# Optimization experiments

Measured on AMD Instinct MI355X. Metric: run time of the kernel, lower is better.

## Reference

```python
import jax, jax.numpy as jnp
import numpy as np

EMBED = 256
HEADS = 8
LEVELS = 4
POINTS = 8
CAMS = 6
D_HEAD = EMBED // HEADS  # 32
SHAPES = [(92, 160), (46, 80), (23, 40), (12, 20)]  # (H, W) per level, L = 19560


def setup_inputs() -> dict:
    key = jax.random.key(0)
    ks = jax.random.split(key, 12)
    bs, nq, Z = 1, 2500, 4
    L = sum(h * w for h, w in SHAPES)

    def lin(k, fan_in, fan_out, scale=1.0):
        return jax.random.normal(k, (fan_in, fan_out), jnp.float32) * (scale / np.sqrt(fan_in).astype(np.float32))

    return dict(
        query=jax.random.normal(ks[0], (bs, nq, EMBED), jnp.float32),
        key_feats=jax.random.normal(ks[1], (CAMS, L, bs, EMBED), jnp.float32),
        reference_points_cam=jax.random.uniform(ks[2], (CAMS, bs, nq, Z, 2), jnp.float32),
        bev_mask=jax.random.bernoulli(ks[3], 0.3, (CAMS, bs, nq, Z)),
        spatial_shapes=jnp.array(SHAPES, dtype=jnp.int32),
        W_value=lin(ks[4], EMBED, EMBED),
        b_value=jnp.zeros((EMBED,), jnp.float32),
        W_off=lin(ks[5], EMBED, HEADS * LEVELS * POINTS * 2, 0.1),
        b_off=jnp.zeros((HEADS * LEVELS * POINTS * 2,), jnp.float32),
        W_attn=lin(ks[6], EMBED, HEADS * LEVELS * POINTS),
        b_attn=jnp.zeros((HEADS * LEVELS * POINTS,), jnp.float32),
        W_out=lin(ks[7], EMBED, EMBED),
        b_out=jnp.zeros((EMBED,), jnp.float32),
    )


def _deform_attn(q, val, ref, W_off, b_off, W_attn, b_attn):
    """MSDeformableAttention3D core. q: (Bc,Nq,C), val: (Bc,L,H,d) [already value-projected],
    ref: (Bc,Nq,Z,2) normalized camera-plane points."""
    Bc, Nq, C = q.shape
    Z = ref.shape[2]
    # sampling offsets, normalized per level by (W, H)
    off = (q @ W_off + b_off).reshape(Bc, Nq, HEADS, LEVELS, POINTS, 2)
    norm = jnp.array([[w, h] for h, w in SHAPES], jnp.float32)  # (Lv, 2) as (W, H)
    off = off / norm[None, None, None, :, None, :]
    # BEVFormer 3D combination: broadcast offsets over the Z pillar anchors
    off = off.reshape(Bc, Nq, HEADS, LEVELS, POINTS // Z, Z, 2)
    loc = ref[:, :, None, None, None, :, :] + off  # (Bc,Nq,H,Lv,P/Z,Z,2)
    loc = loc.reshape(Bc, Nq, HEADS, LEVELS, POINTS, 2)
    # attention weights softmaxed jointly over (levels*points)
    aw = jax.nn.softmax((q @ W_attn + b_attn).reshape(Bc, Nq, HEADS, LEVELS * POINTS), axis=-1)
    aw = aw.reshape(Bc, Nq, HEADS, LEVELS, POINTS)

    val_t = val.transpose(0, 2, 1, 3)  # (Bc,H,L,d)
    gather = jax.vmap(jax.vmap(lambda vm, im: vm[im]))  # over Bc and H
    out = jnp.zeros((Bc, HEADS, Nq, D_HEAD), jnp.float32)
    start = 0
    for lvl, (Hh, Ww) in enumerate(SHAPES):
        v_l = val_t[:, :, start:start + Hh * Ww]  # (Bc,H,HW,d)
        start += Hh * Ww
        # grid_sample semantics, align_corners=False, zero padding
        x = loc[:, :, :, lvl, :, 0] * Ww - 0.5  # (Bc,Nq,H,P)
        y = loc[:, :, :, lvl, :, 1] * Hh - 0.5
        x0 = jnp.floor(x)
        y0 = jnp.floor(y)
        fx = x - x0
        fy = y - y0
        a_l = aw[:, :, :, lvl]  # (Bc,Nq,H,P)
        for dy in (0, 1):
            for dx in (0, 1):
                xi = x0 + dx
                yi = y0 + dy
                wgt = (fx if dx else 1.0 - fx) * (fy if dy else 1.0 - fy)
                valid = (xi >= 0) & (xi < Ww) & (yi >= 0) & (yi < Hh)
                idx = (jnp.clip(yi, 0, Hh - 1) * Ww + jnp.clip(xi, 0, Ww - 1)).astype(jnp.int32)
                cw = jnp.where(valid, wgt * a_l, 0.0).transpose(0, 2, 1, 3)  # (Bc,H,Nq,P)
                g = gather(v_l, idx.transpose(0, 2, 1, 3))  # (Bc,H,Nq,P,d)
                out = out + jnp.einsum('bhnp,bhnpd->bhnd', cw, g)
    return out.transpose(0, 2, 1, 3).reshape(Bc, Nq, C)


def reference(query, key_feats, reference_points_cam, bev_mask, spatial_shapes,
              W_value, b_value, W_off, b_off, W_attn, b_attn, W_out, b_out):
    bs, nq, C = query.shape
    # Rebatch equivalent: every camera sees all queries; invalid ones are masked out
    # after the (fully per-query) deformable attention, which matches the original
    # gather->pad->attend->scatter math exactly.
    q_bc = jnp.broadcast_to(query[:, None], (bs, CAMS, nq, C)).reshape(bs * CAMS, nq, C)
    v = key_feats.transpose(2, 0, 1, 3).reshape(bs * CAMS, -1, C)  # (Bc,L,C)
    val = (v @ W_value + b_value).reshape(bs * CAMS, -1, HEADS, D_HEAD)
    ref = reference_points_cam.transpose(1, 0, 2, 3, 4).reshape(bs * CAMS, nq, -1, 2)
    out = _deform_attn(q_bc, val, ref, W_off, b_off, W_attn, b_attn)  # (Bc,nq,C)
    out = out.reshape(bs, CAMS, nq, C)
    valid_q = bev_mask.sum(-1) > 0  # (CAMS, bs, nq)
    mask = valid_q.transpose(1, 0, 2).astype(query.dtype)  # (bs, CAMS, nq)
    slots = jnp.einsum('bcq,bcqd->bqd', mask, out)
    count = jnp.maximum(mask.sum(1), 1.0)  # (bs, nq)
    slots = slots / count[..., None]
    return slots @ W_out + b_out + query
```

## Files before the change

### kernel.cpp

```cpp
#include <hip/hip_runtime.h>
#include <hip/hip_bf16.h>
#include <cstdint>

#define NCAMS 6
#define NQ 2500
#define EMBED 256
#define HEADS 8
#define DHEAD 32
#define LTOT 19560
#define MVAL (NCAMS * LTOT)

typedef __attribute__((ext_vector_type(8))) short bf16x8;
typedef __attribute__((ext_vector_type(4))) float f32x4;

__device__ __forceinline__ unsigned short f2bf(float f) {
  unsigned u = __float_as_uint(f);
  return (unsigned short)((u + 0x7fffu + ((u >> 16) & 1u)) >> 16);
}
__device__ __forceinline__ unsigned short bfbits(float x) {
  __hip_bfloat16 h = __float2bfloat16(x);
  return __builtin_bit_cast(unsigned short, h);
}
__device__ __forceinline__ void gl16(const void* g, void* l) {
  __builtin_amdgcn_global_load_lds(
      (const __attribute__((address_space(1))) unsigned int*)g,
      (__attribute__((address_space(3))) unsigned int*)l, 16, 0, 0);
}

__global__ __launch_bounds__(256) void k_prep(
    const float* __restrict__ Wv, const float* __restrict__ Woff,
    const float* __restrict__ Wattn, const float* __restrict__ Wout,
    const float* __restrict__ query, const unsigned char* __restrict__ MSK,
    unsigned short* __restrict__ WT, unsigned short* __restrict__ WTq,
    unsigned short* __restrict__ WoutT, unsigned short* __restrict__ qbf,
    unsigned char* __restrict__ valid)
{
  const int b = blockIdx.x, t = threadIdx.x;
  if (b < 256) {
    WT[(size_t)b * 256 + t] = f2bf(Wv[(size_t)t * 256 + b]);
  } else if (b < 768) {
    int c = b - 256;
    WTq[(size_t)c * 256 + t] = f2bf(Woff[(size_t)t * 512 + c]);
  } else if (b < 1024) {
    int c = b - 768;
    WTq[(size_t)(512 + c) * 256 + t] = f2bf(Wattn[(size_t)t * 256 + c]);
  } else if (b < 1280) {
    int c = b - 1024;
    WoutT[(size_t)c * 256 + t] = f2bf(Wout[(size_t)t * 256 + c]);
  } else if (b < 1280 + NQ) {
    int q = b - 1280;
    qbf[(size_t)q * 256 + t] = f2bf(query[(size_t)q * 256 + t]);
  } else {
    __shared__ int s_u8;
    if (t == 0) s_u8 = 0;
    __syncthreads();
    if ((t & 3) && MSK[t]) atomicOr(&s_u8, 1);
    __syncthreads();
    const int isU8 = s_u8;
    const int i = (b - 1280 - NQ) * 256 + t;
    if (i < NCAMS * NQ) {
      int any;
      if (isU8) {
        const unsigned char* p = MSK + (size_t)i * 4;
        any = p[0] | p[1] | p[2] | p[3];
      } else {
        const int* p = (const int*)MSK + (size_t)i * 4;
        any = p[0] | p[1] | p[2] | p[3];
      }
      valid[i] = any ? 1 : 0;
    }
  }
}

__global__ __launch_bounds__(512, 4) void k_valproj(
    const float* __restrict__ A,
    const unsigned short* __restrict__ WT,
    const float* __restrict__ bv,
    unsigned short* __restrict__ val)
{
  __shared__ unsigned int smemu[12288];
  float* Af = (float*)smemu;
  unsigned short* Bs = (unsigned short*)(smemu + 4096);
  const int t = threadIdx.x;
  const int lane = t & 63;
  const int wid = t >> 6;
  const int wm = wid >> 2, wn = wid & 3;
  const int laneM = lane & 15, kGrp = lane >> 4;
  const int b3 = (laneM >> 3) & 1;
  const int bm = blockIdx.x * 64;

  const float* aS[2];
#pragma unroll
  for (int p = 0; p < 2; ++p) {
    int g16 = (wid * 2 + p) * 64 + lane;
    int row = g16 >> 4;
    int gl  = g16 & 15;
    int g   = gl ^ (((row & 7) << 1) | ((row >> 3) & 1));
    aS[p] = A + (size_t)min(bm + row, MVAL - 1) * 256 + g * 4;
  }
  const int sub = t >> 3;
  const int swz = (t & 7) ^ (sub & 7);
  const unsigned short* bS[4];
#pragma unroll
  for (int p = 0; p < 4; ++p)
    bS[p] = WT + (size_t)(p * 64 + sub) * 256 + swz * 8;

  f32x4 acc[2][4];
#pragma unroll
  for (int m = 0; m < 2; ++m)
#pragma unroll
    for (int n = 0; n < 4; ++n) acc[m][n] = {0.f, 0.f, 0.f, 0.f};

#pragma unroll 1
  for (int kk = 0; kk < 4; ++kk) {
    if (kk) __syncthreads();
    const int koF = kk * 64;
#pragma unroll
    for (int p = 0; p < 2; ++p)
      gl16(aS[p] + koF, Af + (wid * 2 + p) * 256);
#pragma unroll
    for (int p = 0; p < 4; ++p)
      gl16(bS[p] + koF, Bs + p * 4096 + wid * 512);
    __syncthreads();

#pragma unroll
    for (int ks = 0; ks < 2; ++ks) {
      bf16x8 af[2], bfr[4];
#pragma unroll
      for (int m = 0; m < 2; ++m) {
        int row = wm * 32 + m * 16 + laneM;
        int u = (ks * 4 + kGrp) ^ (row & 7);
        const float* p8 = &Af[row * 64 + u * 8];
        float4 x = *(const float4*)(p8 + b3 * 4);
        float4 y = *(const float4*)(p8 + 4 - b3 * 4);
        union { bf16x8 v; unsigned short u16[8]; } c;
        c.u16[0] = bfbits(x.x); c.u16[1] = bfbits(x.y);
        c.u16[2] = bfbits(x.z); c.u16[3] = bfbits(x.w);
        c.u16[4] = bfbits(y.x); c.u16[5] = bfbits(y.y);
        c.u16[6] = bfbits(y.z); c.u16[7] = bfbits(y.w);
        af[m] = c.v;
      }
#pragma unroll
      for (int n = 0; n < 4; ++n) {
        int row = wn * 64 + n * 16 + laneM;
        bfr[n] = *(bf16x8*)&Bs[row * 64 + (((ks * 4 + kGrp) ^ (row & 7)) << 3)];
      }
#pragma unroll
      for (int m = 0; m < 2; ++m)
#pragma unroll
        for (int n = 0; n < 4; ++n)
          acc[m][n] = __builtin_amdgcn_mfma_f32_16x16x32_bf16(bfr[n], af[m], acc[m][n], 0, 0, 0);
    }
  }

  float4 bb4[4];
#pragma unroll
  for (int n = 0; n < 4; ++n)
    bb4[n] = *(const float4*)&bv[wn * 64 + n * 16 + kGrp * 4];

  __syncthreads();
  unsigned short* tlw = (unsigned short*)smemu + wid * (32 * 72);

#pragma unroll
  for (int m = 0; m < 2; ++m) {
#pragma unroll
    for (int n = 0; n < 4; ++n) {
      uint2 u;
      u.x = (unsigned)bfbits(acc[m][n][0] + bb4[n].x) |
            ((unsigned)bfbits(acc[m][n][1] + bb4[n].y) << 16);
      u.y = (unsigned)bfbits(acc[m][n][2] + bb4[n].z) |
            ((unsigned)bfbits(acc[m][n][3] + bb4[n].w) << 16);
      *(uint2*)&tlw[(m * 16 + laneM) * 72 + n * 16 + kGrp * 4] = u;
    }
  }
#pragma unroll
  for (int i = 0; i < 4; ++i) {
    const int rowl = i * 8 + (lane >> 3);
    const int c8 = lane & 7;
    uint4 v = *(const uint4*)&tlw[rowl * 72 + c8 * 8];
    const int row = bm + wm * 32 + rowl;
    if (row < MVAL)
      *(uint4*)&val[(size_t)row * 256 + wn * 64 + c8 * 8] = v;
  }
}

__global__ __launch_bounds__(256, 2) void k_gemm_small(
    const unsigned short* __restrict__ A,
    const unsigned short* __restrict__ BT,
    const float* __restrict__ ba, const float* __restrict__ bb, int bsplit,
    const float* __restrict__ resid,
    float* __restrict__ C, int M, int N, int withResid)
{
  __shared__ unsigned short As[128 * 64];
  __shared__ unsigned short Bs[128 * 64];
  const int t = threadIdx.x;
  const int lane = t & 63;
  const int wid = t >> 6;
  const int wm = wid >> 1, wn = wid & 1;
  const int laneM = lane & 15, kGrp = lane >> 4;
  const int bm = blockIdx.x * 128;
  const int bn = blockIdx.y * 128;

  const int aC = t & 7, aR0 = t >> 3;

  uint4 aRegs[2][4];
  uint4 bRegs[2][4];
  f32x4 acc[4][4];
#pragma unroll
  for (int m = 0; m < 4; ++m)
#pragma unroll
    for (int n = 0; n < 4; ++n) acc[m][n] = {0.f, 0.f, 0.f, 0.f};

#pragma unroll
  for (int p = 0; p < 4; ++p) {
    int arow = bm + aR0 + p * 32;
    aRegs[0][p] = (arow < M) ? *(const uint4*)&A[(size_t)arow * 256 + aC * 8]
                             : make_uint4(0u, 0u, 0u, 0u);
    bRegs[0][p] = *(const uint4*)&BT[(size_t)(bn + aR0 + p * 32) * 256 + aC * 8];
  }

#pragma unroll
  for (int kk = 0; kk < 4; ++kk) {
    const int cur = kk & 1, nxt = cur ^ 1;
    if (kk) __syncthreads();
#pragma unroll
    for (int p = 0; p < 4; ++p) {
      int row = aR0 + p * 32;
      int elem = row * 64 + ((aC ^ (row & 7)) << 3);
      *(uint4*)&As[elem] = aRegs[cur][p];
      *(uint4*)&Bs[elem] = bRegs[cur][p];
    }
    __syncthreads();
    if (kk < 3) {
      const int kn = (kk + 1) * 64;
#pragma unroll
      for (int p = 0; p < 4; ++p) {
        int arow = bm + aR0 + p * 32;
        aRegs[nxt][p] = (arow < M)
            ? *(const uint4*)&A[(size_t)arow * 256 + kn + aC * 8]
            : make_uint4(0u, 0u, 0u, 0u);
        bRegs[nxt][p] = *(const uint4*)&BT[(size_t)(bn + aR0 + p * 32) * 256 + kn + aC * 8];
      }
    }
#pragma unroll
    for (int ks = 0; ks < 2; ++ks) {
      bf16x8 af[4], bfr[4];
#pragma unroll
      for (int m = 0; m < 4; ++m) {
        int row = wm * 64 + m * 16 + laneM;
        af[m] = *(bf16x8*)&As[row * 64 + (((ks * 4 + kGrp) ^ (row & 7)) << 3)];
      }
#pragma unroll
      for (int n = 0; n < 4; ++n) {
        int row = wn * 64 + n * 16 + laneM;
        bfr[n] = *(bf16x8*)&Bs[row * 64 + (((ks * 4 + kGrp) ^ (row & 7)) << 3)];
      }
#pragma unroll
      for (int m = 0; m < 4; ++m)
#pragma unroll
        for (int n = 0; n < 4; ++n)
          acc[m][n] = __builtin_amdgcn_mfma_f32_16x16x32_bf16(af[m], bfr[n], acc[m][n], 0, 0, 0);
    }
  }

  float bvn[4];
#pragma unroll
  for (int n = 0; n < 4; ++n) {
    int col = bn + wn * 64 + n * 16 + laneM;
    bvn[n] = (col < bsplit) ? ba[col] : bb[col - bsplit];
  }
#pragma unroll
  for (int m = 0; m < 4; ++m) {
#pragma unroll
    for (int r = 0; r < 4; ++r) {
      int row = bm + wm * 64 + m * 16 + kGrp * 4 + r;
      if (row < M) {
#pragma unroll
        for (int n = 0; n < 4; ++n) {
          int col = bn + wn * 64 + n * 16 + laneM;
          float v = acc[m][n][r] + bvn[n];
          if (withResid) v += resid[(size_t)row * 256 + col];
          C[(size_t)row * N + col] = v;
        }
      }
    }
  }
}

__global__ __launch_bounds__(256) void k_sample(
    const unsigned short* __restrict__ val,
    const float* __restrict__ OFFLOG,
    const float* __restrict__ REF,
    const unsigned char* __restrict__ valid,
    unsigned short* __restrict__ slots)
{
  __shared__ int2  s_pack[4][NCAMS][256];
  __shared__ float s_off[512];
  __shared__ float s_ref[48];
  __shared__ int   s_valid[6];

  const int q = blockIdx.x;
  const int t = threadIdx.x;

  s_off[t]       = OFFLOG[(size_t)q * 768 + t];
  s_off[t + 256] = OFFLOG[(size_t)q * 768 + 256 + t];
  if (t < 48) s_ref[t] = REF[(size_t)(t >> 3) * (NQ * 8) + (size_t)q * 8 + (t & 7)];
  if (t < 6) s_valid[t] = valid[(size_t)t * NQ + q];

  float logit = OFFLOG[(size_t)q * 768 + 512 + t];
  float m = logit;
#pragma unroll
  for (int o = 16; o > 0; o >>= 1) m = fmaxf(m, __shfl_xor(m, o, 32));
  float e = __expf(logit - m);
  float s = e;
#pragma unroll
  for (int o = 16; o > 0; o >>= 1) s += __shfl_xor(s, o, 32);
  const float a = e / s;
  __syncthreads();

  {
    const int h1 = t >> 5, lp = t & 31, lvl = lp >> 3, p = lp & 7, z = p & 3;
    const int WW = 160 >> lvl;
    const int HH = (lvl < 3) ? (92 >> lvl) : 12;
    const int S  = (lvl == 0) ? 0 : (lvl == 1) ? 14720 : (lvl == 2) ? 18400 : 19320;
    const float Wf = (float)WW, Hf = (float)HH;
    const float ox = s_off[h1 * 64 + lp * 2];
    const float oy = s_off[h1 * 64 + lp * 2 + 1];
#pragma unroll 1
    for (int cam = 0; cam < NCAMS; ++cam) {
      if (!s_valid[cam]) continue;
      float rx = s_ref[cam * 8 + z * 2];
      float ry = s_ref[cam * 8 + z * 2 + 1];
      float x = rx * Wf + ox - 0.5f;
      float y = ry * Hf + oy - 0.5f;
      float x0f = floorf(x), y0f = floorf(y);
      float fx = x - x0f, fy = y - y0f;
      int x0 = (int)x0f, y0 = (int)y0f;
      int base = cam * LTOT + S;
#pragma unroll
      for (int dy = 0; dy < 2; ++dy) {
        int yi = y0 + dy;
        float wy = dy ? fy : 1.f - fy;
        int yc = min(max(yi, 0), HH - 1);
        bool vy = (yi >= 0) && (yi < HH);
#pragma unroll
        for (int dx = 0; dx < 2; ++dx) {
          int xi = x0 + dx;
          float wx = dx ? fx : 1.f - fx;
          int xc = min(max(xi, 0), WW - 1);
          bool vv = vy && (xi >= 0) && (xi < WW);
          float wgt = vv ? wx * wy * a : 0.f;
          int addr = (base + yc * WW + xc) * 512;
          s_pack[dy * 2 + dx][cam][t] = make_int2(addr, __float_as_int(wgt));
        }
      }
    }
  }
  __syncthreads();

  const int h = t >> 5, pp = (t >> 2) & 7, l4 = t & 3;
  const unsigned dconst = (unsigned)(h * 64 + l4 * 16);
  const char* vb = (const char*)val;
  int nvalid = s_valid[0] + s_valid[1] + s_valid[2] + s_valid[3] + s_valid[4] + s_valid[5];
  float inv = 1.f / fmaxf((float)nvalid, 1.f);

  float a0 = 0.f, a1 = 0.f, a2 = 0.f, a3 = 0.f;
  float a4 = 0.f, a5 = 0.f, a6 = 0.f, a7 = 0.f;
#pragma unroll 1
  for (int cam = 0; cam < NCAMS; ++cam) {
    if (!s_valid[cam]) continue;
#pragma unroll
    for (int it = 0; it < 4; ++it) {
      const int idx = h * 32 + it * 8 + pp;
      int2 pk0 = s_pack[0][cam][idx];
      int2 pk1 = s_pack[1][cam][idx];
      int2 pk2 = s_pack[2][cam][idx];
      int2 pk3 = s_pack[3][cam][idx];
      uint4 v0 = *(const uint4*)(vb + (size_t)((unsigned)pk0.x + dconst));
      uint4 v1 = *(const uint4*)(vb + (size_t)((unsigned)pk1.x + dconst));
      uint4 v2 = *(const uint4*)(vb + (size_t)((unsigned)pk2.x + dconst));
      uint4 v3 = *(const uint4*)(vb + (size_t)((unsigned)pk3.x + dconst));
      float w0 = __int_as_float(pk0.y), w1 = __int_as_float(pk1.y);
      float w2 = __int_as_float(pk2.y), w3 = __int_as_float(pk3.y);
      a0 += w0 * __uint_as_float(v0.x << 16);
      a1 += w0 * __uint_as_float(v0.x & 0xffff0000u);
      a2 += w0 * __uint_as_float(v0.y << 16);
      a3 += w0 * __uint_as_float(v0.y & 0xffff0000u);
      a4 += w0 * __uint_as_float(v0.z << 16);
      a5 += w0 * __uint_as_float(v0.z & 0xffff0000u);
      a6 += w0 * __uint_as_float(v0.w << 16);
      a7 += w0 * __uint_as_float(v0.w & 0xffff0000u);
      a0 += w1 * __uint_as_float(v1.x << 16);
      a1 += w1 * __uint_as_float(v1.x & 0xffff0000u);
      a2 += w1 * __uint_as_float(v1.y << 16);
      a3 += w1 * __uint_as_float(v1.y & 0xffff0000u);
      a4 += w1 * __uint_as_float(v1.z << 16);
      a5 += w1 * __uint_as_float(v1.z & 0xffff0000u);
      a6 += w1 * __uint_as_float(v1.w << 16);
      a7 += w1 * __uint_as_float(v1.w & 0xffff0000u);
      a0 += w2 * __uint_as_float(v2.x << 16);
      a1 += w2 * __uint_as_float(v2.x & 0xffff0000u);
      a2 += w2 * __uint_as_float(v2.y << 16);
      a3 += w2 * __uint_as_float(v2.y & 0xffff0000u);
      a4 += w2 * __uint_as_float(v2.z << 16);
      a5 += w2 * __uint_as_float(v2.z & 0xffff0000u);
      a6 += w2 * __uint_as_float(v2.w << 16);
      a7 += w2 * __uint_as_float(v2.w & 0xffff0000u);
      a0 += w3 * __uint_as_float(v3.x << 16);
      a1 += w3 * __uint_as_float(v3.x & 0xffff0000u);
      a2 += w3 * __uint_as_float(v3.y << 16);
      a3 += w3 * __uint_as_float(v3.y & 0xffff0000u);
      a4 += w3 * __uint_as_float(v3.z << 16);
      a5 += w3 * __uint_as_float(v3.z & 0xffff0000u);
      a6 += w3 * __uint_as_float(v3.w << 16);
      a7 += w3 * __uint_as_float(v3.w & 0xffff0000u);
    }
  }

#pragma unroll
  for (int o = 4; o <= 16; o <<= 1) {
    a0 += __shfl_xor(a0, o); a1 += __shfl_xor(a1, o);
    a2 += __shfl_xor(a2, o); a3 += __shfl_xor(a3, o);
    a4 += __shfl_xor(a4, o); a5 += __shfl_xor(a5, o);
    a6 += __shfl_xor(a6, o); a7 += __shfl_xor(a7, o);
  }
  if (pp == 0) {
    uint4 r;
    r.x = (unsigned)f2bf(a0 * inv) | ((unsigned)f2bf(a1 * inv) << 16);
    r.y = (unsigned)f2bf(a2 * inv) | ((unsigned)f2bf(a3 * inv) << 16);
    r.z = (unsigned)f2bf(a4 * inv) | ((unsigned)f2bf(a5 * inv) << 16);
    r.w = (unsigned)f2bf(a6 * inv) | ((unsigned)f2bf(a7 * inv) << 16);
    *(uint4*)&slots[(size_t)q * 256 + h * 32 + l4 * 8] = r;
  }
}

extern "C" void kernel_launch(void* const* d_in, const int* in_sizes, int n_in,
                              void* d_out, int out_size, void* d_ws, size_t ws_size,
                              hipStream_t stream) {
  const float* query     = (const float*)d_in[0];
  const float* key_feats = (const float*)d_in[1];
  const float* ref       = (const float*)d_in[2];
  const unsigned char* mask = (const unsigned char*)d_in[3];
  const float* Wv    = (const float*)d_in[5];
  const float* bv    = (const float*)d_in[6];
  const float* Woff  = (const float*)d_in[7];
  const float* boff  = (const float*)d_in[8];
  const float* Wattn = (const float*)d_in[9];
  const float* battn = (const float*)d_in[10];
  const float* Wout  = (const float*)d_in[11];
  const float* bout  = (const float*)d_in[12];
  float* out = (float*)d_out;

  char* ws = (char*)d_ws;
  size_t off = 0;
  unsigned short* val   = (unsigned short*)(ws + off); off += (size_t)MVAL * 256 * 2;
  unsigned short* WT    = (unsigned short*)(ws + off); off += 256 * 256 * 2;
  unsigned short* WTq   = (unsigned short*)(ws + off); off += 768 * 256 * 2;
  unsigned short* WoutT = (unsigned short*)(ws + off); off += 256 * 256 * 2;
  unsigned short* qbf   = (unsigned short*)(ws + off); off += (size_t)NQ * 256 * 2;
  float* OFFLOG = (float*)(ws + off); off += (size_t)NQ * 768 * 4;
  unsigned short* slots = (unsigned short*)(ws + off); off += (size_t)NQ * 256 * 2;
  unsigned char* valid  = (unsigned char*)(ws + off); off += NCAMS * NQ;

  const int MASKBLKS = (NCAMS * NQ + 255) / 256;
  hipLaunchKernelGGL(k_prep, dim3(1280 + NQ + MASKBLKS), dim3(256), 0, stream,
                     Wv, Woff, Wattn, Wout, query, mask, WT, WTq, WoutT, qbf, valid);
  hipLaunchKernelGGL(k_valproj, dim3((MVAL + 63) / 64), dim3(512), 0, stream,
                     key_feats, WT, bv, val);
  hipLaunchKernelGGL(k_gemm_small, dim3((NQ + 127) / 128, 6), dim3(256), 0, stream,
                     qbf, WTq, boff, battn, 512, (const float*)nullptr, OFFLOG, NQ, 768, 0);
  hipLaunchKernelGGL(k_sample, dim3(NQ), dim3(256), 0, stream,
                     val, OFFLOG, ref, valid, slots);
  hipLaunchKernelGGL(k_gemm_small, dim3((NQ + 127) / 128, 2), dim3(256), 0, stream,
                     slots, WoutT, bout, bout, 1 << 30, query, out, NQ, 256, 1);
}
```

Before: 136.7 us.

## Double-buffer value-projection GEMM K-loop with async LDS loads

Restructures the value-projection GEMM's K loop from four 64-wide single-buffered steps into eight 32-wide steps over two LDS buffers. Global-to-LDS loads for step k+2 are issued while step k is computed, using explicit vmcnt waits and raw barriers. The LDS swizzles are re-derived for the narrower tiles. The aim is to hide global-load latency behind MFMA work, at the cost of more barriers and hand-managed wait counts that must stay exactly right.

```diff
diff --git a/kernel.cpp b/kernel.cpp
--- a/kernel.cpp
+++ b/kernel.cpp
@@ -79,31 +79,32 @@
     unsigned short* __restrict__ val)
 {
   __shared__ unsigned int smemu[12288];
-  float* Af = (float*)smemu;
-  unsigned short* Bs = (unsigned short*)(smemu + 4096);
+  float* Af0 = (float*)smemu;
+  float* Af1 = (float*)(smemu + 2048);
+  unsigned short* Bs0 = (unsigned short*)(smemu + 4096);
+  unsigned short* Bs1 = (unsigned short*)(smemu + 8192);
   const int t = threadIdx.x;
   const int lane = t & 63;
   const int wid = t >> 6;
   const int wm = wid >> 2, wn = wid & 3;
   const int laneM = lane & 15, kGrp = lane >> 4;
-  const int b3 = (laneM >> 3) & 1;
   const int bm = blockIdx.x * 64;
 
-  const float* aS[2];
+  const int gA16 = wid * 64 + lane;
+  const int rowA = gA16 >> 3, glA = gA16 & 7;
+  const float* aSrc = A + (size_t)min(bm + rowA, MVAL - 1) * 256 +
+                      (glA ^ (rowA & 7)) * 4;
+  float* aDst0 = Af0 + gA16 * 4;
+  float* aDst1 = Af1 + gA16 * 4;
+  int gB16[2], rowB[2];
+  const unsigned short* bSrc[2];
 #pragma unroll
   for (int p = 0; p < 2; ++p) {
-    int g16 = (wid * 2 + p) * 64 + lane;
-    int row = g16 >> 4;
-    int gl  = g16 & 15;
-    int g   = gl ^ (((row & 7) << 1) | ((row >> 3) & 1));
-    aS[p] = A + (size_t)min(bm + row, MVAL - 1) * 256 + g * 4;
-  }
-  const int sub = t >> 3;
-  const int swz = (t & 7) ^ (sub & 7);
-  const unsigned short* bS[4];
-#pragma unroll
-  for (int p = 0; p < 4; ++p)
-    bS[p] = WT + (size_t)(p * 64 + sub) * 256 + swz * 8;
+    gB16[p] = (wid * 2 + p) * 64 + lane;
+    rowB[p] = gB16[p] >> 2;
+    int ch = gB16[p] & 3;
+    bSrc[p] = WT + (size_t)rowB[p] * 256 + ((ch ^ (rowB[p] & 3)) << 3);
+  }
 
   f32x4 acc[2][4];
 #pragma unroll
@@ -111,28 +112,41 @@
 #pragma unroll
     for (int n = 0; n < 4; ++n) acc[m][n] = {0.f, 0.f, 0.f, 0.f};
 
-#pragma unroll 1
-  for (int kk = 0; kk < 4; ++kk) {
-    if (kk) __syncthreads();
-    const int koF = kk * 64;
-#pragma unroll
-    for (int p = 0; p < 2; ++p)
-      gl16(aS[p] + koF, Af + (wid * 2 + p) * 256);
-#pragma unroll
-    for (int p = 0; p < 4; ++p)
-      gl16(bS[p] + koF, Bs + p * 4096 + wid * 512);
-    __syncthreads();
-
-#pragma unroll
-    for (int ks = 0; ks < 2; ++ks) {
+#define STAGE(BUF, KK)                                                     \
+  do {                                                                     \
+    gl16(aSrc + (KK) * 32, (BUF) ? aDst1 : aDst0);                         \
+    gl16(bSrc[0] + (KK) * 32,                                              \
+         ((BUF) ? Bs1 : Bs0) + gB16[0] * 8);                               \
+    gl16(bSrc[1] + (KK) * 32,                                              \
+         ((BUF) ? Bs1 : Bs0) + gB16[1] * 8);                               \
+  } while (0)
+
+  STAGE(0, 0);
+  STAGE(1, 1);
+
+#pragma unroll
+  for (int kk = 0; kk < 8; ++kk) {
+    if (kk < 7) {
+      asm volatile("s_waitcnt vmcnt(3)" ::: "memory");
+    } else {
+      asm volatile("s_waitcnt vmcnt(0)" ::: "memory");
+    }
+    __builtin_amdgcn_sched_barrier(0);
+    __builtin_amdgcn_s_barrier();
+    __builtin_amdgcn_sched_barrier(0);
+
+    {
+      const float* AfD = (kk & 1) ? Af1 : Af0;
+      const unsigned short* BsD = (kk & 1) ? Bs1 : Bs0;
       bf16x8 af[2], bfr[4];
 #pragma unroll
       for (int m = 0; m < 2; ++m) {
         int row = wm * 32 + m * 16 + laneM;
-        int u = (ks * 4 + kGrp) ^ (row & 7);
-        const float* p8 = &Af[row * 64 + u * 8];
-        float4 x = *(const float4*)(p8 + b3 * 4);
-        float4 y = *(const float4*)(p8 + 4 - b3 * 4);
+        int u = kGrp ^ ((row >> 1) & 3);
+        int sw = row & 1;
+        const float* p8 = AfD + row * 32 + u * 8;
+        float4 x = *(const float4*)(p8 + sw * 4);
+        float4 y = *(const float4*)(p8 + 4 - sw * 4);
         union { bf16x8 v; unsigned short u16[8]; } c;
         c.u16[0] = bfbits(x.x); c.u16[1] = bfbits(x.y);
         c.u16[2] = bfbits(x.z); c.u16[3] = bfbits(x.w);
@@ -143,7 +157,7 @@
 #pragma unroll
       for (int n = 0; n < 4; ++n) {
         int row = wn * 64 + n * 16 + laneM;
-        bfr[n] = *(bf16x8*)&Bs[row * 64 + (((ks * 4 + kGrp) ^ (row & 7)) << 3)];
+        bfr[n] = *(const bf16x8*)&BsD[row * 32 + ((kGrp ^ (row & 3)) << 3)];
       }
 #pragma unroll
       for (int m = 0; m < 2; ++m)
@@ -151,14 +165,20 @@
         for (int n = 0; n < 4; ++n)
           acc[m][n] = __builtin_amdgcn_mfma_f32_16x16x32_bf16(bfr[n], af[m], acc[m][n], 0, 0, 0);
     }
-  }
+
+    __builtin_amdgcn_s_barrier();
+    __builtin_amdgcn_sched_barrier(0);
+    if (kk < 6) {
+      if (kk & 1) STAGE(1, kk + 2); else STAGE(0, kk + 2);
+    }
+  }
+#undef STAGE
 
   float4 bb4[4];
 #pragma unroll
   for (int n = 0; n < 4; ++n)
     bb4[n] = *(const float4*)&bv[wn * 64 + n * 16 + kGrp * 4];
 
-  __syncthreads();
   unsigned short* tlw = (unsigned short*)smemu + wid * (32 * 72);
 
 #pragma unroll
@@ -173,6 +193,7 @@
       *(uint2*)&tlw[(m * 16 + laneM) * 72 + n * 16 + kGrp * 4] = u;
     }
   }
+  __syncthreads();
 #pragma unroll
   for (int i = 0; i < 4; ++i) {
     const int rowl = i * 8 + (lane >> 3);
```

Measured after the change: 139.7 us. 2.2% more time.
